# Kernel optimization log

Hardware: AMD Instinct MI355X
Metric: run time of the kernel (lower is better)

Reference implementation:

```python
import jax, jax.numpy as jnp
import numpy as np
import math

PHI = (1 + math.sqrt(5)) / 2
TABLE_SIZE = 4096
TWO_PI = 2.0 * math.pi
_ang = np.arange(TABLE_SIZE, dtype=np.float32) * (TWO_PI / TABLE_SIZE)
SIN_T = jnp.asarray(np.sin(_ang))
COS_T = jnp.asarray(np.cos(_ang))


def lookup_sin_cos(theta):
    """LUT sin/cos with linear interpolation over a 4096-entry table on [0, 2pi)."""
    pos = (theta / TWO_PI % 1.0) * TABLE_SIZE
    i0f = jnp.floor(pos)
    frac = pos - i0f
    i0 = i0f.astype(jnp.int32) % TABLE_SIZE
    i1 = (i0 + 1) % TABLE_SIZE
    s = SIN_T[i0] * (1.0 - frac) + SIN_T[i1] * frac
    c = COS_T[i0] * (1.0 - frac) + COS_T[i1] * frac
    return s, c


def setup_inputs() -> dict:
    key = jax.random.key(0)
    ks = jax.random.split(key, 8)
    B, S, D, H = 2, 2048, 1024, 16
    dh = D // H
    return {
        "x": jax.random.normal(ks[0], (B, S, D), dtype=jnp.float32),
        "w_q": jax.random.normal(ks[1], (H, dh), dtype=jnp.float32) * 0.02,
        "b_q": jnp.zeros((H, dh), jnp.float32),
        "phi_q": jnp.full((H, dh), PHI, jnp.float32),
        "w_k": jax.random.normal(ks[2], (H, dh), dtype=jnp.float32) * 0.02,
        "b_k": jnp.zeros((H, dh), jnp.float32),
        "phi_k": jnp.full((H, dh), PHI, jnp.float32),
        "w_v": jax.random.normal(ks[3], (H, dh), dtype=jnp.float32) * 0.02,
        "b_v": jnp.zeros((H, dh), jnp.float32),
        "w_out": jax.random.normal(ks[4], (D,), dtype=jnp.float32) * 0.02,
        "b_out": jnp.zeros((D,), jnp.float32),
    }


def reference(x, w_q, b_q, phi_q, w_k, b_k, phi_k, w_v, b_v, w_out, b_out):
    B, S, D = x.shape
    H, dh = w_q.shape
    scale = math.sqrt(2 * dh)
    t = jnp.arange(S, dtype=x.dtype).reshape(1, S, 1, 1)
    xh = x.reshape(B, S, H, dh)

    theta_q = xh / (1.0 + jnp.abs(w_q)) + b_q + t * phi_q
    sin_q, cos_q = lookup_sin_cos(theta_q)
    Q = jnp.concatenate([cos_q, sin_q], axis=-1)  # (B,S,H,2dh)

    theta_k = xh / (1.0 + jnp.abs(w_k)) + b_k + t * phi_k
    sin_k, cos_k = lookup_sin_cos(theta_k)
    K = jnp.concatenate([cos_k, sin_k], axis=-1)  # (B,S,H,2dh)

    theta_v = xh / (1.0 + jnp.abs(w_v)) + b_v
    sin_v, cos_v = lookup_sin_cos(theta_v)
    V = cos_v + sin_v  # (B,S,H,dh)

    scores = jnp.einsum('bqhd,bkhd->bhqk', Q, K) / scale
    causal = jnp.triu(jnp.ones((S, S), dtype=bool), k=1)
    scores = jnp.where(causal, -jnp.inf, scores)
    attn = jax.nn.softmax(scores, axis=-1)
    out = jnp.einsum('bhqk,bkhd->bqhd', attn, V).reshape(B, S, D)

    theta_out = out / (1.0 + jnp.abs(w_out)) + b_out
    sin_o, cos_o = lookup_sin_cos(theta_out)
    return cos_o + sin_o
```

## Files before the change

### kernel.cpp

```cpp
#include <hip/hip_runtime.h>
#include <hip/hip_bf16.h>
#include <math.h>

#define BB 2
#define SS 2048
#define HH 16
#define DH 64
#define DQK 128
#define DD (HH*DH)
#define QS2   0.12751758f
#define EBIAS 11.5415605f

typedef _Float16 half8_t __attribute__((ext_vector_type(8)));
typedef _Float16 half4_t __attribute__((ext_vector_type(4)));
typedef float f32x4_t __attribute__((ext_vector_type(4)));
typedef float f32x4v __attribute__((ext_vector_type(4)));

__device__ __forceinline__ void fsincos(float th, float* sn, float* cs) {
  float rev = th * 0.15915494309189535f;
  rev -= floorf(rev);
#if __has_builtin(__builtin_amdgcn_sinf) && __has_builtin(__builtin_amdgcn_cosf)
  *sn = __builtin_amdgcn_sinf(rev);
  *cs = __builtin_amdgcn_cosf(rev);
#else
  float ang = rev * 6.283185307179586f;
  *sn = __sinf(ang);
  *cs = __cosf(ang);
#endif
}

__device__ __forceinline__ float frcp(float v) {
#if __has_builtin(__builtin_amdgcn_rcpf)
  return __builtin_amdgcn_rcpf(v);
#else
  return 1.f / v;
#endif
}

__global__ __launch_bounds__(256) void gen_qkv(
    const float* __restrict__ x,
    const float* __restrict__ wq, const float* __restrict__ bq,
    const float* __restrict__ phq,
    const float* __restrict__ wk, const float* __restrict__ bk,
    const float* __restrict__ phk,
    const float* __restrict__ wv, const float* __restrict__ bv,
    _Float16* __restrict__ Qd, _Float16* __restrict__ Kd, _Float16* __restrict__ Vtd)
{
  int stile = blockIdx.x >> 5;
  int bh    = blockIdx.x & 31;
  int b = bh >> 4, h = bh & 15;
  int t = threadIdx.x;
  int sl = t >> 2;
  int dq = (t & 3) << 4;
  int s  = stile * 64 + sl;

  __shared__ _Float16 Vl[64 * 65];

  const float* xr = x + (((size_t)b * SS + s) * HH + h) * DH + dq;
  float tv = (float)s;
  int hd0 = h * DH + dq;
  _Float16 qc[16], qs[16], kc[16], ks[16];
#pragma unroll
  for (int g = 0; g < 4; g++) {
    f32x4v x4  = *(const f32x4v*)(xr + g * 4);
    f32x4v wq4 = *(const f32x4v*)(wq + hd0 + g * 4);
    f32x4v bq4 = *(const f32x4v*)(bq + hd0 + g * 4);
    f32x4v pq4 = *(const f32x4v*)(phq + hd0 + g * 4);
    f32x4v wk4 = *(const f32x4v*)(wk + hd0 + g * 4);
    f32x4v bk4 = *(const f32x4v*)(bk + hd0 + g * 4);
    f32x4v pk4 = *(const f32x4v*)(phk + hd0 + g * 4);
    f32x4v wv4 = *(const f32x4v*)(wv + hd0 + g * 4);
    f32x4v bv4 = *(const f32x4v*)(bv + hd0 + g * 4);
#pragma unroll
    for (int i2 = 0; i2 < 4; i2++) {
      int i = g * 4 + i2;
      float xv = x4[i2];
      {
        float th = xv * frcp(1.f + fabsf(wq4[i2])) + fmaf(tv, pq4[i2], bq4[i2]);
        float sn, cs; fsincos(th, &sn, &cs);
        qc[i] = (_Float16)(cs * QS2);
        qs[i] = (_Float16)(sn * QS2);
      }
      {
        float th = xv * frcp(1.f + fabsf(wk4[i2])) + fmaf(tv, pk4[i2], bk4[i2]);
        float sn, cs; fsincos(th, &sn, &cs);
        kc[i] = (_Float16)cs;
        ks[i] = (_Float16)sn;
      }
      {
        float th = xv * frcp(1.f + fabsf(wv4[i2])) + bv4[i2];
        float sn, cs; fsincos(th, &sn, &cs);
        Vl[(dq + i) * 65 + sl] = (_Float16)(cs + sn);
      }
    }
  }
  size_t qbase = ((size_t)bh * SS + s) * DQK;
#pragma unroll
  for (int i = 0; i < 2; i++) {
    *(half8_t*)(Qd + qbase + dq + i * 8)      = *(half8_t*)(&qc[i * 8]);
    *(half8_t*)(Qd + qbase + DH + dq + i * 8) = *(half8_t*)(&qs[i * 8]);
  }
  {
    size_t ktb = ((size_t)bh * 32 + stile) * 8192;
    int fo0 = (t & 3) * 2;
    *(half8_t*)(Kd + ktb + ((size_t)(fo0    ) * 64 + sl) * 8) = *(half8_t*)(&kc[0]);
    *(half8_t*)(Kd + ktb + ((size_t)(fo0 + 1) * 64 + sl) * 8) = *(half8_t*)(&kc[8]);
    *(half8_t*)(Kd + ktb + ((size_t)(fo0 + 8) * 64 + sl) * 8) = *(half8_t*)(&ks[0]);
    *(half8_t*)(Kd + ktb + ((size_t)(fo0 + 9) * 64 + sl) * 8) = *(half8_t*)(&ks[8]);
  }
  __syncthreads();
#pragma unroll
  for (int i = 0; i < 2; i++) {
    int u = t * 2 + i;
    int dv = u & 63, ku = u >> 6;
    _Float16 tmp[8];
#pragma unroll
    for (int jj = 0; jj < 8; jj++) tmp[jj] = Vl[dv * 65 + ku * 8 + jj];
    *(half8_t*)(Vtd + (((size_t)bh * 32 + stile) * 8 + ku) * 512 + dv * 8) =
        *(half8_t*)tmp;
  }
}

__global__ __launch_bounds__(256) void flash_attn(
    const _Float16* __restrict__ Qd, const _Float16* __restrict__ Kd,
    const _Float16* __restrict__ Vtd,
    const float* __restrict__ wout, const float* __restrict__ bout,
    float* __restrict__ out)
{
  int qt = 31 - (blockIdx.x >> 5);
  int bh = blockIdx.x & 31;
  int b  = bh >> 4, hh = bh & 15;
  int nch = qt + 1;
  int q0 = qt * 64;
  int wave = threadIdx.x >> 6;
  int lane = threadIdx.x & 63;
  int lm = lane & 15, lq = lane >> 4;
  int qh = wave >> 1;
  int kh = wave & 1;

  __shared__ __align__(16) float Of[64 * 68];
  __shared__ __align__(16) float Lf[64];

  const _Float16* Kg = Kd + (size_t)bh * 32 * 8192;
  const _Float16* Kw = Kg + ((size_t)lq * 64 + kh * 32 + lm) * 8;
  const _Float16* Vw = Vtd + (size_t)bh * 32 * 4096 +
                       ((size_t)(kh * 4 + (lq >> 1)) * 64 + lm) * 8 + (lq & 1) * 4;

  const _Float16* Qb = Qd + ((size_t)bh * SS + q0 + qh * 32) * DQK;
  half8_t aq[2][4];
#pragma unroll
  for (int qtl = 0; qtl < 2; qtl++)
#pragma unroll
    for (int c = 0; c < 4; c++)
      aq[qtl][c] = *(const half8_t*)(Qb + (qtl * 16 + lm) * DQK + c * 32 + lq * 8);

  f32x4_t o[4][2];
  float l[2] = {0.f, 0.f};
#pragma unroll
  for (int dt = 0; dt < 4; dt++)
#pragma unroll
    for (int qtl = 0; qtl < 2; qtl++) o[dt][qtl] = (f32x4_t){0.f, 0.f, 0.f, 0.f};

  const f32x4_t cinit = (f32x4_t){-EBIAS, -EBIAS, -EBIAS, -EBIAS};

  for (int kt = 0; kt < nch; ++kt) {
    const _Float16* Kc = Kw + (size_t)kt * 8192;
    const _Float16* Vc = Vw + (size_t)kt * 4096;
    int k0 = kt * 64;

    half8_t kf[2][4];
#pragma unroll
    for (int c = 0; c < 4; c++) {
      kf[0][c] = *(const half8_t*)(Kc + (size_t)c * 4 * 64 * 8);
      kf[1][c] = *(const half8_t*)(Kc + (size_t)c * 4 * 64 * 8 + 16 * 8);
    }
    half4_t vr[4][2];
#pragma unroll
    for (int dt = 0; dt < 4; dt++)
#pragma unroll
      for (int kg = 0; kg < 2; kg++)
        vr[dt][kg] = *(const half4_t*)(Vc + ((size_t)kg * 2 * 64 + dt * 16) * 8);

    f32x4_t cST[2][2];
    cST[0][0] = cST[0][1] = cST[1][0] = cST[1][1] = cinit;
#pragma unroll
    for (int c = 0; c < 4; c++) {
      cST[0][0] = __builtin_amdgcn_mfma_f32_16x16x32_f16(kf[0][c], aq[0][c], cST[0][0], 0, 0, 0);
      cST[0][1] = __builtin_amdgcn_mfma_f32_16x16x32_f16(kf[0][c], aq[1][c], cST[0][1], 0, 0, 0);
      cST[1][0] = __builtin_amdgcn_mfma_f32_16x16x32_f16(kf[1][c], aq[0][c], cST[1][0], 0, 0, 0);
      cST[1][1] = __builtin_amdgcn_mfma_f32_16x16x32_f16(kf[1][c], aq[1][c], cST[1][1], 0, 0, 0);
    }

    bool maskit = (kt == nch - 1);
    half4_t pb[2][2];
#pragma unroll
    for (int ktl = 0; ktl < 2; ktl++)
#pragma unroll
      for (int qtl = 0; qtl < 2; qtl++) {
        float pf[4];
#pragma unroll
        for (int r = 0; r < 4; r++) {
          float sv = cST[ktl][qtl][r];
          if (maskit) {
            int key  = k0 + kh * 32 + ktl * 16 + lq * 4 + r;
            int qrow = q0 + qh * 32 + qtl * 16 + lm;
            if (key > qrow) sv = -1e30f;
          }
          pf[r] = __builtin_exp2f(sv);
          l[qtl] += pf[r];
        }
        pb[ktl][qtl] = (half4_t){(_Float16)pf[0], (_Float16)pf[1],
                                 (_Float16)pf[2], (_Float16)pf[3]};
      }

#pragma unroll
    for (int dt = 0; dt < 4; dt++)
#pragma unroll
      for (int kg = 0; kg < 2; kg++) {
        o[dt][0] = __builtin_amdgcn_mfma_f32_16x16x16f16(vr[dt][kg], pb[kg][0], o[dt][0], 0, 0, 0);
        o[dt][1] = __builtin_amdgcn_mfma_f32_16x16x16f16(vr[dt][kg], pb[kg][1], o[dt][1], 0, 0, 0);
      }
  }

#pragma unroll
  for (int qtl = 0; qtl < 2; qtl++) {
    l[qtl] += __shfl_xor(l[qtl], 16);
    l[qtl] += __shfl_xor(l[qtl], 32);
  }

  if (kh == 1) {
#pragma unroll
    for (int qtl = 0; qtl < 2; qtl++) {
      int row = qh * 32 + qtl * 16 + lm;
#pragma unroll
      for (int dt = 0; dt < 4; dt++)
#pragma unroll
        for (int r = 0; r < 4; r++)
          Of[row * 68 + dt * 16 + lq * 4 + r] = o[dt][qtl][r];
      if (lq == 0) Lf[row] = l[qtl];
    }
  }
  __syncthreads();
  if (kh == 0) {
#pragma unroll
    for (int qtl = 0; qtl < 2; qtl++) {
      int row = qh * 32 + qtl * 16 + lm;
      float rl = frcp(l[qtl] + Lf[row]);
#pragma unroll
      for (int dt = 0; dt < 4; dt++)
#pragma unroll
        for (int r = 0; r < 4; r++) {
          int idx = row * 68 + dt * 16 + lq * 4 + r;
          Of[idx] = (o[dt][qtl][r] + Of[idx]) * rl;
        }
    }
  }
  __syncthreads();
  {
    int dcol = hh * DH + lane;
    float iw = frcp(1.f + fabsf(wout[dcol]));
    float bo = bout[dcol];
#pragma unroll
    for (int rr = 0; rr < 16; rr++) {
      int row = wave * 16 + rr;
      float th = Of[row * 68 + lane] * iw + bo;
      float sn, cs; fsincos(th, &sn, &cs);
      out[((size_t)b * SS + q0 + row) * DD + dcol] = cs + sn;
    }
  }
}

extern "C" void kernel_launch(void* const* d_in, const int* in_sizes, int n_in,
                              void* d_out, int out_size, void* d_ws, size_t ws_size,
                              hipStream_t stream) {
  (void)in_sizes; (void)n_in; (void)out_size; (void)ws_size;
  const float* x   = (const float*)d_in[0];
  const float* wq  = (const float*)d_in[1];
  const float* bq  = (const float*)d_in[2];
  const float* phq = (const float*)d_in[3];
  const float* wk  = (const float*)d_in[4];
  const float* bk  = (const float*)d_in[5];
  const float* phk = (const float*)d_in[6];
  const float* wv  = (const float*)d_in[7];
  const float* bv  = (const float*)d_in[8];
  const float* wo  = (const float*)d_in[9];
  const float* bo  = (const float*)d_in[10];

  _Float16* Qd  = (_Float16*)d_ws;
  _Float16* Kd  = Qd + (size_t)BB * HH * SS * DQK;
  _Float16* Vtd = Kd + (size_t)BB * HH * SS * DQK;

  gen_qkv<<<BB * HH * (SS / 64), 256, 0, stream>>>(
      x, wq, bq, phq, wk, bk, phk, wv, bv, Qd, Kd, Vtd);
  flash_attn<<<32 * 32, 256, 0, stream>>>(
      Qd, Kd, Vtd, wo, bo, (float*)d_out);
}
```

Baseline: 148.0 us.

## Split long causal key ranges across blocks with a separate combine kernel

Query tiles with more causal key chunks are split into 2-4 interleaved key-chunk groups, so the attention grid grows from 1024 to 2560 blocks with more even per-block work. Each block writes unnormalized fp16 partial outputs and row sums to a workspace, and a new combine kernel sums the partials, normalizes, and applies the output sin/cos. This relies on the fixed exponent bias, so no running max needs merging. It costs extra workspace traffic, fp16 rounding of the partials, and one more kernel launch.

```diff
diff --git a/kernel.cpp b/kernel.cpp
--- a/kernel.cpp
+++ b/kernel.cpp
@@ -10,6 +10,7 @@
 #define DD (HH*DH)
 #define QS2   0.12751758f
 #define EBIAS 11.5415605f
+#define SLOTP 4352
 
 typedef _Float16 half8_t __attribute__((ext_vector_type(8)));
 typedef _Float16 half4_t __attribute__((ext_vector_type(4)));
@@ -123,13 +124,16 @@
 
 __global__ __launch_bounds__(256) void flash_attn(
     const _Float16* __restrict__ Qd, const _Float16* __restrict__ Kd,
-    const _Float16* __restrict__ Vtd,
-    const float* __restrict__ wout, const float* __restrict__ bout,
-    float* __restrict__ out)
+    const _Float16* __restrict__ Vtd, _Float16* __restrict__ Pd)
 {
-  int qt = 31 - (blockIdx.x >> 5);
   int bh = blockIdx.x & 31;
-  int b  = bh >> 4, hh = bh & 15;
+  int o_ = blockIdx.x >> 5;
+  int gidx = (o_ < 32) ? (79 - o_) : ((o_ < 40) ? (39 - o_) : (87 - o_));
+  int qt, g, ng, cnt;
+  if (gidx >= 48)      { int r = gidx - 48; qt = 24 + (r >> 2); g = r & 3; ng = 4; cnt = (qt + 1 - g + 3) >> 2; }
+  else if (gidx >= 24) { int r = gidx - 24; int d3 = (r * 11) >> 5;  qt = 16 + d3; g = r - 3 * d3; ng = 3; cnt = (qt + 1 - g + 2) / 3; }
+  else if (gidx >= 8)  { int r = gidx - 8;  qt = 8 + (r >> 1); g = r & 1; ng = 2; cnt = (qt + 1 - g + 1) >> 1; }
+  else                 { qt = gidx; g = 0; ng = 1; cnt = qt + 1; }
   int nch = qt + 1;
   int q0 = qt * 64;
   int wave = threadIdx.x >> 6;
@@ -141,8 +145,8 @@
   __shared__ __align__(16) float Of[64 * 68];
   __shared__ __align__(16) float Lf[64];
 
-  const _Float16* Kg = Kd + (size_t)bh * 32 * 8192;
-  const _Float16* Kw = Kg + ((size_t)lq * 64 + kh * 32 + lm) * 8;
+  const _Float16* Kw = Kd + (size_t)bh * 32 * 8192 +
+                       ((size_t)lq * 64 + kh * 32 + lm) * 8;
   const _Float16* Vw = Vtd + (size_t)bh * 32 * 4096 +
                        ((size_t)(kh * 4 + (lq >> 1)) * 64 + lm) * 8 + (lq & 1) * 4;
 
@@ -163,7 +167,8 @@
 
   const f32x4_t cinit = (f32x4_t){-EBIAS, -EBIAS, -EBIAS, -EBIAS};
 
-  for (int kt = 0; kt < nch; ++kt) {
+  for (int i = 0; i < cnt; ++i) {
+    int kt = g + i * ng;
     const _Float16* Kc = Kw + (size_t)kt * 8192;
     const _Float16* Vc = Vw + (size_t)kt * 4096;
     int k0 = kt * 64;
@@ -242,31 +247,67 @@
   }
   __syncthreads();
   if (kh == 0) {
+    _Float16* sp = Pd + (size_t)(bh * 80 + gidx) * SLOTP;
+    float* lp = (float*)(sp + 4096);
 #pragma unroll
     for (int qtl = 0; qtl < 2; qtl++) {
-      int row = qh * 32 + qtl * 16 + lm;
-      float rl = frcp(l[qtl] + Lf[row]);
+      int qg = qh * 32 + qtl * 16 + lm;
 #pragma unroll
       for (int dt = 0; dt < 4; dt++)
 #pragma unroll
         for (int r = 0; r < 4; r++) {
-          int idx = row * 68 + dt * 16 + lq * 4 + r;
-          Of[idx] = (o[dt][qtl][r] + Of[idx]) * rl;
+          int dv = dt * 16 + lq * 4 + r;
+          sp[dv * 64 + qg] = (_Float16)(o[dt][qtl][r] + Of[qg * 68 + dv]);
         }
-    }
-  }
+      if (lq == 0) lp[qg] = l[qtl] + Lf[qg];
+    }
+  }
+}
+
+__global__ __launch_bounds__(256) void combine(
+    const _Float16* __restrict__ Pd,
+    const float* __restrict__ wout, const float* __restrict__ bout,
+    float* __restrict__ out)
+{
+  int qt = blockIdx.x >> 5;
+  int bh = blockIdx.x & 31;
+  int b = bh >> 4, hh = bh & 15;
+  int band = qt >> 3;
+  int ng = band + 1;
+  int base = bh * 80 + ((band * (band + 1)) >> 1) * 8 + (qt & 7) * ng;
+  int t = threadIdx.x;
+  int q = t & 63;
+  int dvb = t >> 6;
+
+  float acc[16];
+#pragma unroll
+  for (int i = 0; i < 16; i++) acc[i] = 0.f;
+  float lv = 0.f;
+  for (int gi = 0; gi < ng; gi++) {
+    const _Float16* sp = Pd + (size_t)(base + gi) * SLOTP;
+    lv += ((const float*)(sp + 4096))[q];
+#pragma unroll
+    for (int i = 0; i < 16; i++)
+      acc[i] += (float)sp[(dvb * 16 + i) * 64 + q];
+  }
+  float rl = frcp(lv);
+
+  __shared__ float Osh[64 * 65];
+#pragma unroll
+  for (int i = 0; i < 16; i++)
+    Osh[q * 65 + dvb * 16 + i] = acc[i] * rl;
   __syncthreads();
-  {
-    int dcol = hh * DH + lane;
-    float iw = frcp(1.f + fabsf(wout[dcol]));
-    float bo = bout[dcol];
-#pragma unroll
-    for (int rr = 0; rr < 16; rr++) {
-      int row = wave * 16 + rr;
-      float th = Of[row * 68 + lane] * iw + bo;
-      float sn, cs; fsincos(th, &sn, &cs);
-      out[((size_t)b * SS + q0 + row) * DD + dcol] = cs + sn;
-    }
+
+  int dv2 = t & 63;
+  int dcol = hh * DH + dv2;
+  float iw = frcp(1.f + fabsf(wout[dcol]));
+  float bo = bout[dcol];
+#pragma unroll
+  for (int r = 0; r < 16; r++) {
+    int qrow = (t >> 6) + r * 4;
+    float th = Osh[qrow * 65 + dv2] * iw + bo;
+    float sn, cs; fsincos(th, &sn, &cs);
+    out[((size_t)b * SS + qt * 64 + qrow) * DD + dcol] = cs + sn;
   }
 }
 
@@ -289,9 +330,10 @@
   _Float16* Qd  = (_Float16*)d_ws;
   _Float16* Kd  = Qd + (size_t)BB * HH * SS * DQK;
   _Float16* Vtd = Kd + (size_t)BB * HH * SS * DQK;
+  _Float16* Pd  = Vtd + (size_t)BB * HH * SS * DH;
 
   gen_qkv<<<BB * HH * (SS / 64), 256, 0, stream>>>(
       x, wq, bq, phq, wk, bk, phk, wv, bv, Qd, Kd, Vtd);
-  flash_attn<<<32 * 32, 256, 0, stream>>>(
-      Qd, Kd, Vtd, wo, bo, (float*)d_out);
-}
+  flash_attn<<<80 * 32, 256, 0, stream>>>(Qd, Kd, Vtd, Pd);
+  combine<<<32 * 32, 256, 0, stream>>>(Pd, wo, bo, (float*)d_out);
+}
```

Result: slower. 156.1 us (+5.5%).
